# Optimization experiments

Hardware: AMD Instinct MI355X
Metric: run time of the kernel (lower is better)

Reference implementation:

```python
import jax, jax.numpy as jnp
import numpy as np

N = 131072   # n_nodes == n_edges (required by the broadcast in the original module)
C = 256      # node_channels == edge_channels (required by the broadcast)
EPS_BN = 1e-5
EPS = 1e-5


def _linear_params(key, out_c, in_c):
    k1, k2 = jax.random.split(key)
    bound = 1.0 / np.sqrt(in_c)
    W = jax.random.uniform(k1, (out_c, in_c), minval=-bound, maxval=bound, dtype=jnp.float32)
    b = jax.random.uniform(k2, (out_c,), minval=-bound, maxval=bound, dtype=jnp.float32)
    return W, b


def setup_inputs() -> dict:
    key = jax.random.key(0)
    ks = jax.random.split(key, 10)
    h = jax.random.normal(ks[0], (N, C), dtype=jnp.float32)
    e = jax.random.normal(ks[1], (N, C), dtype=jnp.float32)
    edge_index = jax.random.randint(ks[2], (2, N), 0, N, dtype=jnp.int64)
    A_w, A_b = _linear_params(ks[3], C, C)
    B_w, B_b = _linear_params(ks[4], C, C)
    C_w, C_b = _linear_params(ks[5], C, C)
    D_w, D_b = _linear_params(ks[6], C, C)
    U_w, U_b = _linear_params(ks[7], C, C)
    V_w, V_b = _linear_params(ks[8], C, C)
    bn_gamma = jnp.ones((C,), dtype=jnp.float32)
    bn_beta = jnp.zeros((C,), dtype=jnp.float32)
    return dict(h=h, edge_index=edge_index, e=e,
                A_w=A_w, A_b=A_b, B_w=B_w, B_b=B_b,
                C_w=C_w, C_b=C_b, D_w=D_w, D_b=D_b,
                bn_gamma=bn_gamma, bn_beta=bn_beta,
                U_w=U_w, U_b=U_b, V_w=V_w, V_b=V_b)


def reference(h, edge_index, e,
              A_w, A_b, B_w, B_b, C_w, C_b, D_w, D_b,
              bn_gamma, bn_beta, U_w, U_b, V_w, V_b):
    row, col = edge_index[0], edge_index[1]
    # gather + four parallel linears, summed: [E, C]
    e_out = (h[row] @ A_w.T + A_b
             + h[col] @ B_w.T + B_b
             + e[col] @ C_w.T + C_b
             + e[row] @ D_w.T + D_b)
    # BatchNorm1d (training mode: batch stats, biased variance) + ReLU
    mu = jnp.mean(e_out, axis=0)
    var = jnp.var(e_out, axis=0)
    e_out = jax.nn.relu(bn_gamma * (e_out - mu) * jax.lax.rsqrt(var + EPS_BN) + bn_beta)
    # scatter-add edge messages into node-indexed e, then sigmoid-normalize over dim 0
    e_new = e.at[row].add(e_out)
    e_new = jax.nn.sigmoid(e_new)
    e_new = e_new / (jnp.sum(e_new, axis=0, keepdims=True) + EPS)
    # final gather-multiply-reduce: (e_new * V(h[col])).sum(0) broadcasts [N,C]*[E,C] with N==E
    h_out = h @ U_w.T + U_b + jnp.sum(e_new * (h[col] @ V_w.T + V_b), axis=0)
    h_out = jax.nn.relu(h_out)
    return h_out, e_new
```

## Files before the change

kernel.cpp:

```cpp
#include <hip/hip_runtime.h>
#include <hip/hip_bf16.h>


typedef __attribute__((ext_vector_type(8))) short bf16x8;
typedef __attribute__((ext_vector_type(4))) float f32x4;

__device__ __forceinline__ float b2f(unsigned int lo16) {
  union { unsigned int u; float f; } c; c.u = lo16 << 16; return c.f;
}
__device__ __forceinline__ float lof(unsigned int u) { return b2f(u & 0xffffu); }
__device__ __forceinline__ float hif(unsigned int u) { return b2f(u >> 16); }
__device__ __forceinline__ unsigned int f2b(float f) {
  union { float f; unsigned int u; } c; c.f = f;
  unsigned int u = c.u;
  u += 0x7fffu + ((u >> 16) & 1u);
  return u >> 16;
}

__device__ __forceinline__ void prep_chunk(const float* __restrict__ src,
                                           unsigned short* __restrict__ dst, int g) {
  int mtile = g >> 9;
  int rem = g & 511;
  int r = rem >> 5, k8 = rem & 31;
  const float4* s = reinterpret_cast<const float4*>(src + (((size_t)mtile * 16 + r) << 8) + k8 * 8);
  float4 v0 = s[0], v1 = s[1];
  uint4 o;
  o.x = f2b(v0.x) | (f2b(v0.y) << 16);
  o.y = f2b(v0.z) | (f2b(v0.w) << 16);
  o.z = f2b(v1.x) | (f2b(v1.y) << 16);
  o.w = f2b(v1.z) | (f2b(v1.w) << 16);
  *reinterpret_cast<uint4*>(dst + ((size_t)mtile * 512 + k8 * 16 + r) * 8) = o;
}

__global__ __launch_bounds__(256) void prep_he(const float* __restrict__ h,
                                               unsigned short* __restrict__ h_t,
                                               const float* __restrict__ e,
                                               unsigned short* __restrict__ e_t,
                                               int nChunksEach) {
  int g = blockIdx.x * 256 + threadIdx.x;
  if (g < nChunksEach) prep_chunk(h, h_t, g);
  else if (g < 2 * nChunksEach) prep_chunk(e, e_t, g - nChunksEach);
}

__global__ __launch_bounds__(256) void prep_weights(
    const float* __restrict__ s0, const float* __restrict__ s1,
    const float* __restrict__ s2, const float* __restrict__ s3,
    const float* __restrict__ s4, const float* __restrict__ s5,
    unsigned short* __restrict__ W1h, unsigned short* __restrict__ W1e,
    unsigned short* __restrict__ W2t,
    const float* __restrict__ Ab, const float* __restrict__ Db,
    const float* __restrict__ Bb, const float* __restrict__ Cb,
    const float* __restrict__ Vb, const float* __restrict__ Ub,
    float* __restrict__ b1, float* __restrict__ b2,
    float* __restrict__ sums, float* __restrict__ sumsq,
    float* __restrict__ colsum, float* __restrict__ Traw,
    const int* __restrict__ ei, int* __restrict__ mode) {
  int g = blockIdx.x * 256 + threadIdx.x;
  if (blockIdx.x == 0) {
    const int t = threadIdx.x;
    b1[t] = Ab[t] + Db[t];
    b1[256 + t] = Bb[t] + Cb[t];
    b2[t] = Vb[t];
    b2[256 + t] = Ub[t];
    sums[t] = 0.f; sumsq[t] = 0.f; colsum[t] = 0.f; Traw[t] = 0.f;
    if (t == 0) {
      int m = 0;
#pragma unroll
      for (int i = 1; i < 64; i += 2) m |= ei[i];
      *mode = (m == 0) ? 1 : 0;
    }
  }
  int sel = g >> 13;
  int gg = g & 8191;
  const float* src; unsigned short* dst;
  switch (sel) {
    case 0: src = s0; dst = W1h; break;
    case 1: src = s1; dst = W1h + 65536; break;
    case 2: src = s2; dst = W1e; break;
    case 3: src = s3; dst = W1e + 65536; break;
    case 4: src = s4; dst = W2t; break;
    default: src = s5; dst = W2t + 65536; break;
  }
  prep_chunk(src, dst, gg);
}

__global__ __launch_bounds__(256) void gemm_bt2(
    const unsigned short* __restrict__ Ah, const unsigned short* __restrict__ Ae,
    const unsigned short* __restrict__ Bh, const unsigned short* __restrict__ Be,
    const float* __restrict__ bias, unsigned short* __restrict__ Cmat,
    int O, int nColBlk, int ktSteps, int nBlk) {
  __shared__ char lds[32768];
  const int cpx = nBlk >> 3;
  const int hw = blockIdx.x;
  const int bid = (hw % 8) * cpx + hw / 8;
  const int colBlk = bid % nColBlk;
  const int rowBlk = bid / nColBlk;
  const int tid = threadIdx.x;
  const int w = tid >> 6, lane = tid & 63;
  const int wm = w >> 1, wn = w & 1;

  const size_t aTileOff = (size_t)(rowBlk * 8 + w * 2) * 8192 + lane * 16;
  const size_t bTileOff = (size_t)(colBlk * 8 + w * 2) * 8192 + lane * 16;
  const int wOff0 = (w * 2) * 1024;
  const int wOff1 = (w * 2 + 1) * 1024;

  f32x4 acc[4][4] = {};

  auto stage = [&](int kt, char* bufA, char* bufB) {
    const char* Ab_ = (const char*)(kt < 8 ? Ah : Ae) + aTileOff + (size_t)(kt & 7) * 1024;
    const char* Bb_ = (const char*)(kt < 8 ? Bh : Be) + bTileOff + (size_t)(kt & 7) * 1024;
    __builtin_amdgcn_global_load_lds((const __attribute__((address_space(1))) void*)Ab_,
                                     (__attribute__((address_space(3))) void*)(bufA + wOff0), 16, 0, 0);
    __builtin_amdgcn_global_load_lds((const __attribute__((address_space(1))) void*)(Ab_ + 8192),
                                     (__attribute__((address_space(3))) void*)(bufA + wOff1), 16, 0, 0);
    __builtin_amdgcn_global_load_lds((const __attribute__((address_space(1))) void*)Bb_,
                                     (__attribute__((address_space(3))) void*)(bufB + wOff0), 16, 0, 0);
    __builtin_amdgcn_global_load_lds((const __attribute__((address_space(1))) void*)(Bb_ + 8192),
                                     (__attribute__((address_space(3))) void*)(bufB + wOff1), 16, 0, 0);
  };
  auto compute = [&](const char* bufA, const char* bufB) {
    bf16x8 a[4], b[4];
#pragma unroll
    for (int mi = 0; mi < 4; ++mi)
      a[mi] = *reinterpret_cast<const bf16x8*>(bufA + (wm * 4 + mi) * 1024 + lane * 16);
#pragma unroll
    for (int ni = 0; ni < 4; ++ni)
      b[ni] = *reinterpret_cast<const bf16x8*>(bufB + (wn * 4 + ni) * 1024 + lane * 16);
#pragma unroll
    for (int mi = 0; mi < 4; ++mi)
#pragma unroll
      for (int ni = 0; ni < 4; ++ni)
        acc[mi][ni] = __builtin_amdgcn_mfma_f32_16x16x32_bf16(a[mi], b[ni], acc[mi][ni], 0, 0, 0);
  };

  char* A0 = lds;          char* A1 = lds + 8192;
  char* B0 = lds + 16384;  char* B1 = lds + 24576;

  stage(0, A0, B0);
  __syncthreads();
#pragma unroll 1
  for (int kt = 0; kt < ktSteps; kt += 2) {
    stage(kt + 1, A1, B1);
    compute(A0, B0);
    __syncthreads();
    if (kt + 2 < ktSteps) stage(kt + 2, A0, B0);
    compute(A1, B1);
    __syncthreads();
  }

  const int rb = rowBlk * 128 + wm * 64 + ((lane >> 4) << 2);
  const int cb = colBlk * 128 + wn * 64 + (lane & 15);
#pragma unroll
  for (int mi = 0; mi < 4; ++mi) {
#pragma unroll
    for (int ni = 0; ni < 4; ++ni) {
      const int coln = cb + ni * 16;
      const float bz = bias[coln];
      const size_t base = (size_t)(rb + mi * 16) * O + coln;
#pragma unroll
      for (int r = 0; r < 4; ++r)
        Cmat[base + (size_t)r * O] = (unsigned short)f2b(acc[mi][ni][r] + bz);
    }
  }
}

__global__ __launch_bounds__(256) void edge_stats(
    const unsigned short* __restrict__ PRPC,
    const int* __restrict__ rows_s, const int* __restrict__ cols_s,
    float* __restrict__ sums, float* __restrict__ sumsq) {
  __shared__ float red[8][256];
  const int c8 = threadIdx.x & 31;
  const int sub = threadIdx.x >> 5;
  float s[8], q[8];
#pragma unroll
  for (int j = 0; j < 8; ++j) { s[j] = 0.f; q[j] = 0.f; }
#pragma unroll 1
  for (int grp = 0; grp < 2; ++grp) {
    const int kb = blockIdx.x * 64 + grp * 32 + sub * 4;
    int r[4], cj[4];
#pragma unroll
    for (int u = 0; u < 4; ++u) { r[u] = rows_s[kb + u]; cj[u] = cols_s[kb + u]; }
    uint4 pr[4], pc[4];
#pragma unroll
    for (int u = 0; u < 4; ++u)
      pr[u] = *reinterpret_cast<const uint4*>(PRPC + (size_t)r[u] * 512 + c8 * 8);
#pragma unroll
    for (int u = 0; u < 4; ++u)
      pc[u] = *reinterpret_cast<const uint4*>(PRPC + (size_t)cj[u] * 512 + 256 + c8 * 8);
#pragma unroll
    for (int u = 0; u < 4; ++u) {
      const unsigned int rw[4] = {pr[u].x, pr[u].y, pr[u].z, pr[u].w};
      const unsigned int cw[4] = {pc[u].x, pc[u].y, pc[u].z, pc[u].w};
#pragma unroll
      for (int p4 = 0; p4 < 4; ++p4) {
        const float v0 = lof(rw[p4]) + lof(cw[p4]);
        const float v1 = hif(rw[p4]) + hif(cw[p4]);
        s[2 * p4] += v0;     q[2 * p4] += v0 * v0;
        s[2 * p4 + 1] += v1; q[2 * p4 + 1] += v1 * v1;
      }
    }
  }
#pragma unroll
  for (int j = 0; j < 8; ++j) red[sub][c8 * 8 + j] = s[j];
  __syncthreads();
  {
    const int c = threadIdx.x;
    float t = 0.f;
#pragma unroll
    for (int u2 = 0; u2 < 8; ++u2) t += red[u2][c];
    atomicAdd(sums + c, t);
  }
  __syncthreads();
#pragma unroll
  for (int j = 0; j < 8; ++j) red[sub][c8 * 8 + j] = q[j];
  __syncthreads();
  {
    const int c = threadIdx.x;
    float t = 0.f;
#pragma unroll
    for (int u2 = 0; u2 < 8; ++u2) t += red[u2][c];
    atomicAdd(sumsq + c, t);
  }
}

__global__ __launch_bounds__(256) void hist_rows(const int* __restrict__ ei,
                                                 const int* __restrict__ modep,
                                                 int* __restrict__ cnt, int Nn) {
  const int k = blockIdx.x * 256 + threadIdx.x;
  if (k >= Nn) return;
  const int row = (*modep) ? ei[2 * k] : ei[k];
  atomicAdd(&cnt[row], 1);
}

__global__ __launch_bounds__(256) void scan1(const int* __restrict__ cnt,
                                             int* __restrict__ bsum) {
  __shared__ int red[256];
  const int t = threadIdx.x;
  red[t] = cnt[blockIdx.x * 256 + t];
  __syncthreads();
#pragma unroll
  for (int s = 128; s > 0; s >>= 1) {
    if (t < s) red[t] += red[t + s];
    __syncthreads();
  }
  if (t == 0) bsum[blockIdx.x] = red[0];
}

__global__ __launch_bounds__(512) void scan2(int* __restrict__ bsum, int nb) {
  __shared__ int tmp[512];
  const int t = threadIdx.x;
  const int own = (t < nb) ? bsum[t] : 0;
  tmp[t] = own;
  __syncthreads();
  for (int off = 1; off < 512; off <<= 1) {
    int v = (t >= off) ? tmp[t - off] : 0;
    __syncthreads();
    tmp[t] += v;
    __syncthreads();
  }
  if (t < nb) bsum[t] = tmp[t] - own;
}

__global__ __launch_bounds__(256) void scan3(const int* __restrict__ cnt,
                                             const int* __restrict__ bsum,
                                             int* __restrict__ base, int Nn) {
  __shared__ int tmp[256];
  const int t = threadIdx.x;
  const int gid = blockIdx.x * 256 + t;
  const int own = cnt[gid];
  tmp[t] = own;
  __syncthreads();
  for (int off = 1; off < 256; off <<= 1) {
    int v = (t >= off) ? tmp[t - off] : 0;
    __syncthreads();
    tmp[t] += v;
    __syncthreads();
  }
  base[gid] = tmp[t] - own + bsum[blockIdx.x];
  if (gid == 0) base[Nn] = Nn;
}

__global__ __launch_bounds__(256) void scatter_eids(const int* __restrict__ ei,
                                                    const int* __restrict__ modep,
                                                    const int* __restrict__ base,
                                                    int* __restrict__ cnt,
                                                    int* __restrict__ rows_s,
                                                    int* __restrict__ cols_s, int Nn) {
  const int k = blockIdx.x * 256 + threadIdx.x;
  if (k >= Nn) return;
  int row, col;
  if (*modep) { row = ei[2 * k]; col = ei[2 * (Nn + k)]; }
  else        { row = ei[k];     col = ei[Nn + k]; }
  const int pos = base[row] + atomicAdd(&cnt[row], -1) - 1;
  rows_s[pos] = row;
  cols_s[pos] = col;
}

#define GCAP 1024
__global__ __launch_bounds__(256) void gather_sig_T(
    const float* __restrict__ e, const unsigned short* __restrict__ PRPC,
    const int* __restrict__ base, const int* __restrict__ cols_s,
    const int* __restrict__ ei, const int* __restrict__ modep,
    const unsigned short* __restrict__ VU,
    const float* __restrict__ sums, const float* __restrict__ sumsq,
    const float* __restrict__ gamma, const float* __restrict__ beta,
    unsigned short* __restrict__ accB, float* __restrict__ colsum,
    float* __restrict__ Traw, float invE, int Nn) {
  __shared__ float red[4][256];
  __shared__ int colsL[GCAP];
  __shared__ int baseL[65];
  const int lane = threadIdx.x & 63, w = threadIdx.x >> 6;
  const int n0 = blockIdx.x * 64;
  if (threadIdx.x < 65) baseL[threadIdx.x] = base[n0 + threadIdx.x];
  __syncthreads();
  const int bstart = baseL[0];
  const int bcount = baseL[64] - bstart;
  for (int qq = threadIdx.x; qq < bcount && qq < GCAP; qq += 256)
    colsL[qq] = cols_s[bstart + qq];
  const float4 sm = *reinterpret_cast<const float4*>(sums + lane * 4);
  const float4 sq = *reinterpret_cast<const float4*>(sumsq + lane * 4);
  const float4 gm = *reinterpret_cast<const float4*>(gamma + lane * 4);
  const float4 bt = *reinterpret_cast<const float4*>(beta + lane * 4);
  float4 sc, sh;
  {
    const float mx = sm.x * invE, my = sm.y * invE, mz = sm.z * invE, mw = sm.w * invE;
    sc.x = gm.x * rsqrtf(fmaxf(sq.x * invE - mx * mx, 0.f) + 1e-5f);
    sc.y = gm.y * rsqrtf(fmaxf(sq.y * invE - my * my, 0.f) + 1e-5f);
    sc.z = gm.z * rsqrtf(fmaxf(sq.z * invE - mz * mz, 0.f) + 1e-5f);
    sc.w = gm.w * rsqrtf(fmaxf(sq.w * invE - mw * mw, 0.f) + 1e-5f);
    sh.x = bt.x - mx * sc.x; sh.y = bt.y - my * sc.y;
    sh.z = bt.z - mz * sc.z; sh.w = bt.w - mw * sc.w;
  }
  __syncthreads();
  const int mode = *modep;
  float s0 = 0.f, s1 = 0.f, s2 = 0.f, s3 = 0.f;
  float t0 = 0.f, t1 = 0.f, t2 = 0.f, t3 = 0.f;
  const int i0 = n0 + w * 16;
  int p = baseL[w * 16];
  const int pendW = baseL[w * 16 + 16];
  uint2 pcn; pcn.x = 0; pcn.y = 0;
  if (p < pendW) {
    const int q0 = p - bstart;
    const int cj = (q0 < GCAP) ? colsL[q0] : cols_s[p];
    pcn = *reinterpret_cast<const uint2*>(PRPC + (size_t)cj * 512 + 256 + lane * 4);
  }
  float4 ev = *reinterpret_cast<const float4*>(e + (size_t)i0 * 256 + lane * 4);
  uint2 prv = *reinterpret_cast<const uint2*>(PRPC + (size_t)i0 * 512 + lane * 4);
#pragma unroll 1
  for (int it = 0; it < 16; ++it) {
    const int i = i0 + it;
    const int colT = mode ? ei[2 * (Nn + i)] : ei[Nn + i];
    const uint2 hv = *reinterpret_cast<const uint2*>(VU + (size_t)colT * 512 + lane * 4);
    float4 v = ev;
    const uint2 pr = prv;
    if (it + 1 < 16) {
      ev = *reinterpret_cast<const float4*>(e + (size_t)(i + 1) * 256 + lane * 4);
      prv = *reinterpret_cast<const uint2*>(PRPC + (size_t)(i + 1) * 512 + lane * 4);
    }
    const float pr0 = lof(pr.x), pr1 = hif(pr.x), pr2 = lof(pr.y), pr3 = hif(pr.y);
    const int pe = baseL[w * 16 + it + 1];
#pragma unroll 1
    while (p < pe) {
      const uint2 pc = pcn;
      if (p + 1 < pendW) {
        const int qn = p + 1 - bstart;
        const int cj = (qn < GCAP) ? colsL[qn] : cols_s[p + 1];
        pcn = *reinterpret_cast<const uint2*>(PRPC + (size_t)cj * 512 + 256 + lane * 4);
      }
      v.x += fmaxf(fmaf(sc.x, pr0 + lof(pc.x), sh.x), 0.f);
      v.y += fmaxf(fmaf(sc.y, pr1 + hif(pc.x), sh.y), 0.f);
      v.z += fmaxf(fmaf(sc.z, pr2 + lof(pc.y), sh.z), 0.f);
      v.w += fmaxf(fmaf(sc.w, pr3 + hif(pc.y), sh.w), 0.f);
      ++p;
    }
    v.x = 1.f / (1.f + __expf(-v.x));
    v.y = 1.f / (1.f + __expf(-v.y));
    v.z = 1.f / (1.f + __expf(-v.z));
    v.w = 1.f / (1.f + __expf(-v.w));
    uint2 ob;
    ob.x = f2b(v.x) | (f2b(v.y) << 16);
    ob.y = f2b(v.z) | (f2b(v.w) << 16);
    *reinterpret_cast<uint2*>(accB + (size_t)i * 256 + lane * 4) = ob;
    s0 += v.x; s1 += v.y; s2 += v.z; s3 += v.w;
    t0 += v.x * lof(hv.x); t1 += v.y * hif(hv.x);
    t2 += v.z * lof(hv.y); t3 += v.w * hif(hv.y);
  }
  red[w][lane * 4 + 0] = s0;
  red[w][lane * 4 + 1] = s1;
  red[w][lane * 4 + 2] = s2;
  red[w][lane * 4 + 3] = s3;
  __syncthreads();
  {
    const int c = threadIdx.x;
    atomicAdd(colsum + c, red[0][c] + red[1][c] + red[2][c] + red[3][c]);
  }
  __syncthreads();
  red[w][lane * 4 + 0] = t0;
  red[w][lane * 4 + 1] = t1;
  red[w][lane * 4 + 2] = t2;
  red[w][lane * 4 + 3] = t3;
  __syncthreads();
  {
    const int c = threadIdx.x;
    atomicAdd(Traw + c, red[0][c] + red[1][c] + red[2][c] + red[3][c]);
  }
}

__global__ __launch_bounds__(256) void finalize(
    const unsigned short* __restrict__ accB, const unsigned short* __restrict__ VU,
    const float* __restrict__ colsum, const float* __restrict__ Traw,
    float* __restrict__ outE, float* __restrict__ outH, int nChunks) {
  const int g = blockIdx.x * 256 + threadIdx.x;
  if (g >= nChunks) return;
  const int i = g >> 5, c8 = g & 31;
  const float4 cs0 = *reinterpret_cast<const float4*>(colsum + c8 * 8);
  const float4 cs1 = *reinterpret_cast<const float4*>(colsum + c8 * 8 + 4);
  const float4 tr0 = *reinterpret_cast<const float4*>(Traw + c8 * 8);
  const float4 tr1 = *reinterpret_cast<const float4*>(Traw + c8 * 8 + 4);
  float iv[8] = {1.f / (cs0.x + 1e-5f), 1.f / (cs0.y + 1e-5f),
                 1.f / (cs0.z + 1e-5f), 1.f / (cs0.w + 1e-5f),
                 1.f / (cs1.x + 1e-5f), 1.f / (cs1.y + 1e-5f),
                 1.f / (cs1.z + 1e-5f), 1.f / (cs1.w + 1e-5f)};
  float tt[8] = {tr0.x * iv[0], tr0.y * iv[1], tr0.z * iv[2], tr0.w * iv[3],
                 tr1.x * iv[4], tr1.y * iv[5], tr1.z * iv[6], tr1.w * iv[7]};
  const uint4 sb = *reinterpret_cast<const uint4*>(accB + (size_t)i * 256 + c8 * 8);
  const unsigned int sw[4] = {sb.x, sb.y, sb.z, sb.w};
  float4 e0, e1;
  e0.x = lof(sw[0]) * iv[0]; e0.y = hif(sw[0]) * iv[1];
  e0.z = lof(sw[1]) * iv[2]; e0.w = hif(sw[1]) * iv[3];
  e1.x = lof(sw[2]) * iv[4]; e1.y = hif(sw[2]) * iv[5];
  e1.z = lof(sw[3]) * iv[6]; e1.w = hif(sw[3]) * iv[7];
  float4* qe = reinterpret_cast<float4*>(outE + (size_t)i * 256 + c8 * 8);
  qe[0] = e0; qe[1] = e1;
  const uint4 hu = *reinterpret_cast<const uint4*>(VU + (size_t)i * 512 + 256 + c8 * 8);
  float4 o0, o1;
  o0.x = fmaxf(lof(hu.x) + tt[0], 0.f);
  o0.y = fmaxf(hif(hu.x) + tt[1], 0.f);
  o0.z = fmaxf(lof(hu.y) + tt[2], 0.f);
  o0.w = fmaxf(hif(hu.y) + tt[3], 0.f);
  o1.x = fmaxf(lof(hu.z) + tt[4], 0.f);
  o1.y = fmaxf(hif(hu.z) + tt[5], 0.f);
  o1.z = fmaxf(lof(hu.w) + tt[6], 0.f);
  o1.w = fmaxf(hif(hu.w) + tt[7], 0.f);
  float4* qh = reinterpret_cast<float4*>(outH + (size_t)i * 256 + c8 * 8);
  qh[0] = o0; qh[1] = o1;
}

extern "C" void kernel_launch(void* const* d_in, const int* in_sizes, int n_in,
                              void* d_out, int out_size, void* d_ws, size_t ws_size,
                              hipStream_t stream) {
  const float* h     = (const float*)d_in[0];
  const int*   ei    = (const int*)d_in[1];
  const float* e     = (const float*)d_in[2];
  const float* Aw    = (const float*)d_in[3];
  const float* Ab    = (const float*)d_in[4];
  const float* Bw    = (const float*)d_in[5];
  const float* Bb    = (const float*)d_in[6];
  const float* Cw    = (const float*)d_in[7];
  const float* Cb    = (const float*)d_in[8];
  const float* Dw    = (const float*)d_in[9];
  const float* Db    = (const float*)d_in[10];
  const float* gamma = (const float*)d_in[11];
  const float* beta  = (const float*)d_in[12];
  const float* Uw    = (const float*)d_in[13];
  const float* Ub    = (const float*)d_in[14];
  const float* Vw    = (const float*)d_in[15];
  const float* Vb    = (const float*)d_in[16];
  const int N = in_sizes[0] / 256;

  char* ws = (char*)d_ws;
  unsigned short* W1h = (unsigned short*)(ws + 0x0);
  unsigned short* W1e = (unsigned short*)(ws + 0x40000);
  unsigned short* W2t = (unsigned short*)(ws + 0x80000);
  float* b1     = (float*)(ws + 0xC0000);
  float* b2     = (float*)(ws + 0xC0800);
  float* sums   = (float*)(ws + 0xC1000);
  float* sumsq  = (float*)(ws + 0xC1400);
  float* colsum = (float*)(ws + 0xC1800);
  float* Traw   = (float*)(ws + 0xC1C00);
  int*   mode   = (int*)(ws + 0xC2C00);
  unsigned short* h_t  = (unsigned short*)(ws + 0x100000);
  unsigned short* e_t  = (unsigned short*)(ws + 0x4100000);
  unsigned short* PRPC = (unsigned short*)(ws + 0x8100000);
  unsigned short* VU   = (unsigned short*)(ws + 0x10100000);
  unsigned short* accB = (unsigned short*)(ws + 0x100000);
  int* cnt    = (int*)(ws + 0x18100000);
  int* baseA  = (int*)(ws + 0x18180000);
  int* rows_s = (int*)(ws + 0x18210000);
  int* cols_s = (int*)(ws + 0x18290000);
  int* bsum   = (int*)(ws + 0x18310000);

  float* outH = (float*)d_out;
  float* outE = outH + (size_t)N * 256;

  hipMemsetAsync(cnt, 0, (size_t)N * 4, stream);
  prep_weights<<<192, 256, 0, stream>>>(Aw, Bw, Dw, Cw, Vw, Uw, W1h, W1e, W2t,
                                        Ab, Db, Bb, Cb, Vb, Ub, b1, b2,
                                        sums, sumsq, colsum, Traw, ei, mode);

  hist_rows<<<N / 256, 256, 0, stream>>>(ei, mode, cnt, N);
  scan1<<<N / 256, 256, 0, stream>>>(cnt, bsum);
  scan2<<<1, 512, 0, stream>>>(bsum, N / 256);
  scan3<<<N / 256, 256, 0, stream>>>(cnt, bsum, baseA, N);
  scatter_eids<<<N / 256, 256, 0, stream>>>(ei, mode, baseA, cnt, rows_s, cols_s, N);

  const int nChunks = N * 32;
  prep_he<<<2 * nChunks / 256, 256, 0, stream>>>(h, h_t, e, e_t, nChunks);
  gemm_bt2<<<(N / 128) * 4, 256, 0, stream>>>(h_t, e_t, W1h, W1e, b1, PRPC, 512, 4, 16, (N / 128) * 4);
  gemm_bt2<<<(N / 128) * 4, 256, 0, stream>>>(h_t, h_t, W2t, W2t, b2, VU, 512, 4, 8, (N / 128) * 4);

  edge_stats<<<N / 64, 256, 0, stream>>>(PRPC, rows_s, cols_s, sums, sumsq);
  gather_sig_T<<<N / 64, 256, 0, stream>>>(e, PRPC, baseA, cols_s, ei, mode, VU,
                                           sums, sumsq, gamma, beta,
                                           accB, colsum, Traw, 1.0f / (float)N, N);
  finalize<<<nChunks / 256, 256, 0, stream>>>(accB, VU, colsum, Traw, outE, outH, nChunks);
}
```

Before: 582.7 us.

## Triple-buffer GEMM LDS staging with one barrier per k-step

Replaces the double-buffered LDS pipeline in the bf16 GEMM with a three-stage ring buffer. Loads are kept two k-steps ahead, partial vmcnt waits replace the full drain, and only one barrier runs per iteration instead of two. The goal is to hide global-to-LDS latency and cut synchronisation stalls. In exchange LDS use per block grows from 32 KB to 48 KB, which may lower occupancy, and the hand-written waitcnt logic relies on the compiler issuing exactly four loads per stage.

```diff
diff --git a/kernel.cpp b/kernel.cpp
--- a/kernel.cpp
+++ b/kernel.cpp
@@ -89,7 +89,7 @@
     const unsigned short* __restrict__ Bh, const unsigned short* __restrict__ Be,
     const float* __restrict__ bias, unsigned short* __restrict__ Cmat,
     int O, int nColBlk, int ktSteps, int nBlk) {
-  __shared__ char lds[32768];
+  __shared__ char lds[49152];
   const int cpx = nBlk >> 3;
   const int hw = blockIdx.x;
   const int bid = (hw % 8) * cpx + hw / 8;
@@ -118,7 +118,7 @@
     __builtin_amdgcn_global_load_lds((const __attribute__((address_space(1))) void*)(Bb_ + 8192),
                                      (__attribute__((address_space(3))) void*)(bufB + wOff1), 16, 0, 0);
   };
-  auto compute = [&](const char* bufA, const char* bufB) {
+  auto computeFrom = [&](const char* bufA, const char* bufB) {
     bf16x8 a[4], b[4];
 #pragma unroll
     for (int mi = 0; mi < 4; ++mi)
@@ -133,19 +133,28 @@
         acc[mi][ni] = __builtin_amdgcn_mfma_f32_16x16x32_bf16(a[mi], b[ni], acc[mi][ni], 0, 0, 0);
   };
 
-  char* A0 = lds;          char* A1 = lds + 8192;
-  char* B0 = lds + 16384;  char* B1 = lds + 24576;
+  char* A0 = lds;          char* A1 = lds + 8192;   char* A2 = lds + 16384;
+  char* B0 = lds + 24576;  char* B1 = lds + 32768;  char* B2 = lds + 40960;
 
   stage(0, A0, B0);
-  __syncthreads();
+  stage(1, A1, B1);
+  char *Ac = A0, *An = A1, *Aq = A2;
+  char *Bc = B0, *Bn = B1, *Bq = B2;
+
 #pragma unroll 1
-  for (int kt = 0; kt < ktSteps; kt += 2) {
-    stage(kt + 1, A1, B1);
-    compute(A0, B0);
-    __syncthreads();
-    if (kt + 2 < ktSteps) stage(kt + 2, A0, B0);
-    compute(A1, B1);
-    __syncthreads();
+  for (int kt = 0; kt < ktSteps; ++kt) {
+    if (kt + 1 < ktSteps) {
+      asm volatile("s_waitcnt vmcnt(4)" ::: "memory");
+    } else {
+      asm volatile("s_waitcnt vmcnt(0)" ::: "memory");
+    }
+    __builtin_amdgcn_s_barrier();
+    asm volatile("" ::: "memory");
+    __builtin_amdgcn_sched_barrier(0);
+    if (kt + 2 < ktSteps) stage(kt + 2, Aq, Bq);
+    computeFrom(Ac, Bc);
+    char* tA = Ac; Ac = An; An = Aq; Aq = tA;
+    char* tB = Bc; Bc = Bn; Bn = Bq; Bq = tB;
   }
 
   const int rb = rowBlk * 128 + wm * 64 + ((lane >> 4) << 2);
```

Result: faster. 539.6 us, median of 2 (-7.4%).
